# Kernel optimization log

Measured on AMD Instinct MI355X. Metric: run time of the kernel, lower is better.

Reference implementation:

```python
import jax, jax.numpy as jnp
import numpy as np

B, N, FIN, FOUT = 8, 2048, 128, 128


def setup_inputs() -> dict:
    key = jax.random.key(0)
    k1, k2, k3, k4, k5 = jax.random.split(key, 5)
    x = jax.random.normal(k1, (B, N, FIN), dtype=jnp.float32)
    adj = jax.random.randint(k2, (N, N), 0, 2, dtype=jnp.int32)
    # W stored [in, out] (transpose of torch Linear weight; same math via x @ W)
    W = jax.random.normal(k3, (FIN, FOUT), dtype=jnp.float32) * (1.0 / np.sqrt(FIN))
    # a: Linear(2*out, 1) split into src/dst halves: a([h_i,h_j]) = h_i@a_src + h_j@a_dst
    a_src = jax.random.normal(k4, (FOUT,), dtype=jnp.float32) * 0.1
    a_dst = jax.random.normal(k5, (FOUT,), dtype=jnp.float32) * 0.1
    return {"x": x, "adj": adj, "W": W, "a_src": a_src, "a_dst": a_dst}


def reference(x, adj, W, a_src, a_dst):
    # h: [B, N, FOUT]
    h = jnp.einsum('bnf,fo->bno', x, W)
    # attention logits e_ij = LeakyReLU(a_src.h_i + a_dst.h_j), built by broadcast
    s_i = jnp.einsum('bno,o->bn', h, a_src)  # [B, N]
    s_j = jnp.einsum('bno,o->bn', h, a_dst)  # [B, N]
    e = jax.nn.leaky_relu(s_i[:, :, None] + s_j[:, None, :], negative_slope=0.2)  # [B,N,N]
    scores = jnp.where(adj[None, :, :] == 0, -jnp.inf, e)
    attn = jax.nn.softmax(scores, axis=-1)
    attn = jnp.nan_to_num(attn, nan=0.0)  # rows with no neighbors -> all zeros
    # dropout is identity in eval mode
    out = jnp.einsum('bij,bjo->bio', attn, h)  # [B, N, FOUT]
    return out
```

## Files before the change

### kernel.cpp

```cpp
#include <hip/hip_runtime.h>
#include <math.h>

#define BATCH 8
#define NN 2048
#define FF 128

typedef __attribute__((ext_vector_type(4))) float f32x4;
typedef _Float16 half8 __attribute__((ext_vector_type(8)));

__device__ __forceinline__ unsigned short h2u(_Float16 h) {
    return __builtin_bit_cast(unsigned short, h);
}

__global__ __launch_bounds__(256) void k_h(const float* __restrict__ x,
                                           const int* __restrict__ adj,
                                           const float* __restrict__ W,
                                           const float* __restrict__ a_src,
                                           const float* __restrict__ a_dst,
                                           unsigned short* __restrict__ hF,
                                           float* __restrict__ Eg,  float* __restrict__ E2g,
                                           float* __restrict__ Sg,  float* __restrict__ S2g,
                                           unsigned* __restrict__ amT) {
    __shared__ float sred[4 * 16];
    __shared__ float dred[4 * 16];

    const int t = threadIdx.x;
    const int w = t >> 6, lane = t & 63;
    const int nl = lane & 15, quad = lane >> 4;
    const int row0 = blockIdx.x * 16;
    const int b = row0 >> 11, jloc0 = row0 & 2047;
    const int gr = row0 + nl;
    const int nt0 = w * 2;

    {
        const int prow = blockIdx.x * 2 + (w >> 1);
        const int* __restrict__ ar = adj + (size_t)prow * NN;
        const int s0 = (w & 1) * 16;
        #pragma unroll
        for (int s = 0; s < 16; ++s) {
            const int seg = s0 + s;
            const unsigned long long m = __ballot(ar[seg * 64 + lane] != 0);
            if (lane == 0)  amT[(size_t)(seg * 2) * NN + prow] = (unsigned)m;
            if (lane == 32) amT[(size_t)(seg * 2 + 1) * NN + prow] = (unsigned)(m >> 32);
        }
    }

    f32x4 acc[2] = {{0.f,0.f,0.f,0.f},{0.f,0.f,0.f,0.f}};

    #pragma unroll
    for (int ks = 0; ks < 4; ++ks) {
        const float4 xa = *reinterpret_cast<const float4*>(&x[(size_t)gr * FF + ks * 32 + quad * 8]);
        const float4 xb = *reinterpret_cast<const float4*>(&x[(size_t)gr * FF + ks * 32 + quad * 8 + 4]);
        const float xv[8] = {xa.x, xa.y, xa.z, xa.w, xb.x, xb.y, xb.z, xb.w};
        half8 ah, al;
        #pragma unroll
        for (int i = 0; i < 8; ++i) {
            const _Float16 hh = (_Float16)xv[i];
            ah[i] = hh;
            al[i] = (_Float16)(xv[i] - (float)hh);
        }
        #pragma unroll
        for (int nn = 0; nn < 2; ++nn) {
            const float* __restrict__ wp = W + (size_t)(ks * 32 + quad * 8) * FF + (nt0 + nn) * 16 + nl;
            half8 bh, bl;
            #pragma unroll
            for (int j = 0; j < 8; ++j) {
                const float wv = wp[j * FF];
                const _Float16 hh = (_Float16)wv;
                bh[j] = hh;
                bl[j] = (_Float16)(wv - (float)hh);
            }
            acc[nn] = __builtin_amdgcn_mfma_f32_16x16x32_f16(ah, bh, acc[nn], 0, 0, 0);
            acc[nn] = __builtin_amdgcn_mfma_f32_16x16x32_f16(al, bh, acc[nn], 0, 0, 0);
            acc[nn] = __builtin_amdgcn_mfma_f32_16x16x32_f16(ah, bl, acc[nn], 0, 0, 0);
        }
    }

    const int jloc = jloc0 + quad * 4;
    const int jg = jloc >> 3, u0 = jloc & 7;
    #pragma unroll
    for (int nn = 0; nn < 2; ++nn) {
        ushort4 hv;
        hv.x = h2u((_Float16)acc[nn][0]);
        hv.y = h2u((_Float16)acc[nn][1]);
        hv.z = h2u((_Float16)acc[nn][2]);
        hv.w = h2u((_Float16)acc[nn][3]);
        *reinterpret_cast<ushort4*>(&hF[(size_t)b * 262144 + (nt0 + nn) * 32768 + jg * 128 + nl * 8 + u0]) = hv;
    }

    float as[2], ad[2];
    #pragma unroll
    for (int nn = 0; nn < 2; ++nn) {
        const int col = (nt0 + nn) * 16 + nl;
        as[nn] = a_src[col];
        ad[nn] = a_dst[col];
    }
    #pragma unroll
    for (int r = 0; r < 4; ++r) {
        float sp = acc[0][r] * as[0] + acc[1][r] * as[1];
        float dp = acc[0][r] * ad[0] + acc[1][r] * ad[1];
        #pragma unroll
        for (int off = 8; off >= 1; off >>= 1) {
            sp += __shfl_xor(sp, off, 16);
            dp += __shfl_xor(dp, off, 16);
        }
        if (nl == 0) {
            sred[w * 16 + quad * 4 + r] = sp;
            dred[w * 16 + quad * 4 + r] = dp;
        }
    }
    __syncthreads();
    if (t < 16) {
        const float sp = sred[t] + sred[16 + t] + sred[32 + t] + sred[48 + t];
        const float dp = dred[t] + dred[16 + t] + dred[32 + t] + dred[48 + t];
        const int row = row0 + t;
        Sg[row]  = __expf(sp - 2.f);
        S2g[row] = __expf(0.2f * sp - 2.f);
        Eg[row]  = __expf(dp - 2.f);
        E2g[row] = __expf(0.2f * dp - 2.f);
    }
}

__global__ __launch_bounds__(512, 4) void k_attn(const unsigned short* __restrict__ hF,
                                                 const unsigned* __restrict__ amT,
                                                 const float* __restrict__ Eg,
                                                 const float* __restrict__ E2g,
                                                 const float* __restrict__ Sg,
                                                 const float* __restrict__ S2g,
                                                 float* __restrict__ P,
                                                 float* __restrict__ L) {
    __shared__ float E_l[512];
    __shared__ float E2_l[512];
    __shared__ unsigned am_l[16 * 64];
    __shared__ unsigned short pA[2 * 64 * 72];

    const int t = threadIdx.x;
    const int b = blockIdx.y;
    const int i0 = blockIdx.x * 64;
    const int jh = blockIdx.z;
    const int jbase = jh * 512;

    E_l[t]  = Eg[(size_t)b * NN + jbase + t];
    E2_l[t] = E2g[(size_t)b * NN + jbase + t];
    #pragma unroll
    for (int k = 0; k < 2; ++k) {
        const int idx = k * 512 + t;
        am_l[idx] = amT[(size_t)(jh * 16 + (idx >> 6)) * NN + i0 + (idx & 63)];
    }
    __syncthreads();

    const int rp = t >> 4, jw4 = t & 15;
    const int ra = rp * 2, rb = ra + 1;
    const float Sa  = Sg[(size_t)b * NN + i0 + ra];
    const float S2a = S2g[(size_t)b * NN + i0 + ra];
    const float Sb  = Sg[(size_t)b * NN + i0 + rb];
    const float S2b = S2g[(size_t)b * NN + i0 + rb];
    const int bitb = (jw4 & 7) * 4;
    const int pwo = ra * 72 + jw4 * 4;

    const int w = t >> 6, lane = t & 63;
    const int nl = lane & 15, quad = lane >> 4;
    const int mtp = w & 1, ntp = w >> 1;
    const unsigned short* __restrict__ hFb = hF + (size_t)b * 262144;
    int bofs[2], aofs[2];
    #pragma unroll
    for (int nn = 0; nn < 2; ++nn) bofs[nn] = (ntp + nn * 4) * 32768 + (jbase + quad * 8) * 16 + nl * 8;
    #pragma unroll
    for (int mm = 0; mm < 2; ++mm) aofs[mm] = ((mtp + mm * 2) * 16 + nl) * 72 + quad * 8;

    f32x4 acc[2][2] = {{{0.f,0.f,0.f,0.f},{0.f,0.f,0.f,0.f}},{{0.f,0.f,0.f,0.f},{0.f,0.f,0.f,0.f}}};
    f32x4 lac[2] = {{0.f,0.f,0.f,0.f},{0.f,0.f,0.f,0.f}};
    half8 ones;
    #pragma unroll
    for (int i = 0; i < 8; ++i) ones[i] = (_Float16)1.f;

    for (int tt = 0; tt < 8; ++tt) {
        const int buf = tt & 1;
        const int jofs = tt * 1024;

        half8 bfr[2][2];
        #pragma unroll
        for (int nn = 0; nn < 2; ++nn) {
            bfr[nn][0] = *reinterpret_cast<const half8*>(hFb + bofs[nn] + jofs);
            bfr[nn][1] = *reinterpret_cast<const half8*>(hFb + bofs[nn] + jofs + 512);
        }

        {
            const int jb = tt * 64 + jw4 * 4;
            const float4 ej4  = *reinterpret_cast<const float4*>(&E_l[jb]);
            const float4 e2j4 = *reinterpret_cast<const float4*>(&E2_l[jb]);
            const uint2 mw = *reinterpret_cast<const uint2*>(&am_l[(tt * 2 + (jw4 >> 3)) * 64 + ra]);
            const float ejA[4]  = {ej4.x, ej4.y, ej4.z, ej4.w};
            const float e2jA[4] = {e2j4.x, e2j4.y, e2j4.z, e2j4.w};
            ushort4 ha, hb;
            #pragma unroll
            for (int jj = 0; jj < 4; ++jj) {
                const float ua = fmaxf(Sa * ejA[jj], S2a * e2jA[jj]);
                const float ub = fmaxf(Sb * ejA[jj], S2b * e2jA[jj]);
                const float pa = ((mw.x >> (bitb + jj)) & 1u) ? ua : 0.f;
                const float pb = ((mw.y >> (bitb + jj)) & 1u) ? ub : 0.f;
                ((unsigned short*)&ha)[jj] = h2u((_Float16)pa);
                ((unsigned short*)&hb)[jj] = h2u((_Float16)pb);
            }
            *reinterpret_cast<ushort4*>(&pA[buf * 4608 + pwo]) = ha;
            *reinterpret_cast<ushort4*>(&pA[buf * 4608 + pwo + 72]) = hb;
        }

        __syncthreads();

        half8 afr[2][2];
        #pragma unroll
        for (int mm = 0; mm < 2; ++mm) {
            afr[mm][0] = *reinterpret_cast<const half8*>(&pA[buf * 4608 + aofs[mm]]);
            afr[mm][1] = *reinterpret_cast<const half8*>(&pA[buf * 4608 + aofs[mm] + 32]);
        }
        #pragma unroll
        for (int mm = 0; mm < 2; ++mm) {
            #pragma unroll
            for (int kh = 0; kh < 2; ++kh) {
                lac[mm] = __builtin_amdgcn_mfma_f32_16x16x32_f16(afr[mm][kh], ones, lac[mm], 0, 0, 0);
                acc[mm][0] = __builtin_amdgcn_mfma_f32_16x16x32_f16(afr[mm][kh], bfr[0][kh], acc[mm][0], 0, 0, 0);
                acc[mm][1] = __builtin_amdgcn_mfma_f32_16x16x32_f16(afr[mm][kh], bfr[1][kh], acc[mm][1], 0, 0, 0);
            }
        }
    }

    float* __restrict__ Pb = P + ((size_t)jh * BATCH + b) * 262144;
    float* __restrict__ Lb = L + ((size_t)jh * BATCH + b) * 2048;
    #pragma unroll
    for (int mm = 0; mm < 2; ++mm) {
        const int lrow = (mtp + mm * 2) * 16 + quad * 4;
        #pragma unroll
        for (int r = 0; r < 4; ++r) {
            #pragma unroll
            for (int nn = 0; nn < 2; ++nn) {
                const int col = (ntp + nn * 4) * 16 + nl;
                Pb[(size_t)(i0 + lrow + r) * FF + col] = acc[mm][nn][r];
            }
            if (nl == 0 && ntp == 0) Lb[i0 + lrow + r] = lac[mm][r];
        }
    }
}

__global__ __launch_bounds__(256) void k_comb(const float* __restrict__ P,
                                              const float* __restrict__ L,
                                              float* __restrict__ out) {
    const int g0 = blockIdx.x * 512 + threadIdx.x;
    #pragma unroll
    for (int it = 0; it < 2; ++it) {
        const int g = g0 + it * 256;
        const size_t flat = (size_t)g * 4;
        const int row = (int)(flat >> 7);
        const float l = L[row] + L[16384 + row] + L[32768 + row] + L[49152 + row];
        const float inv = (l > 0.f) ? 1.f / l : 0.f;
        const float4 p0 = *reinterpret_cast<const float4*>(&P[flat]);
        const float4 p1 = *reinterpret_cast<const float4*>(&P[2097152 + flat]);
        const float4 p2 = *reinterpret_cast<const float4*>(&P[4194304 + flat]);
        const float4 p3 = *reinterpret_cast<const float4*>(&P[6291456 + flat]);
        *reinterpret_cast<float4*>(&out[flat]) =
            make_float4((p0.x + p1.x + p2.x + p3.x) * inv,
                        (p0.y + p1.y + p2.y + p3.y) * inv,
                        (p0.z + p1.z + p2.z + p3.z) * inv,
                        (p0.w + p1.w + p2.w + p3.w) * inv);
    }
}

extern "C" void kernel_launch(void* const* d_in, const int* in_sizes, int n_in,
                              void* d_out, int out_size, void* d_ws, size_t ws_size,
                              hipStream_t stream) {
    const float* x     = (const float*)d_in[0];
    const int*   adj   = (const int*)d_in[1];
    const float* W     = (const float*)d_in[2];
    const float* a_src = (const float*)d_in[3];
    const float* a_dst = (const float*)d_in[4];
    float* out = (float*)d_out;

    unsigned short* hF = (unsigned short*)d_ws;
    float* Eg  = (float*)(hF + 2097152);
    float* E2g = Eg + 16384;
    float* Sg  = E2g + 16384;
    float* S2g = Sg + 16384;
    unsigned* amT = (unsigned*)(S2g + 16384);
    float* P = (float*)(amT + 131072);
    float* L = P + 8388608;

    k_h<<<1024, 256, 0, stream>>>(x, adj, W, a_src, a_dst, hF, Eg, E2g, Sg, S2g, amT);
    k_attn<<<dim3(32, BATCH, 4), 512, 0, stream>>>(hF, amT, Eg, E2g, Sg, S2g, P, L);
    k_comb<<<1024, 256, 0, stream>>>(P, L, out);
}
```

Baseline: 113.8 us.

## Halve the j-split, read E/mask from global, compute row sums with shuffles

The attention kernel now splits the neighbour dimension into 2 chunks instead of 4, so each block loops over 16 tiles, and the partial P/L buffers and the combine pass shrink to two slices. The LDS staging of E, E2 and the adjacency mask is dropped in favour of direct global loads inside the loop, which also removes the initial barrier. Row sums are accumulated in scalar registers and reduced with 16-lane shuffles instead of an extra MFMA against a ones vector. The trade-off is half as many blocks (512), giving less parallelism, plus global-load latency inside the loop.

```diff
diff --git a/kernel.cpp b/kernel.cpp
--- a/kernel.cpp
+++ b/kernel.cpp
@@ -129,25 +129,13 @@
                                                  const float* __restrict__ S2g,
                                                  float* __restrict__ P,
                                                  float* __restrict__ L) {
-    __shared__ float E_l[512];
-    __shared__ float E2_l[512];
-    __shared__ unsigned am_l[16 * 64];
     __shared__ unsigned short pA[2 * 64 * 72];
 
     const int t = threadIdx.x;
     const int b = blockIdx.y;
     const int i0 = blockIdx.x * 64;
     const int jh = blockIdx.z;
-    const int jbase = jh * 512;
-
-    E_l[t]  = Eg[(size_t)b * NN + jbase + t];
-    E2_l[t] = E2g[(size_t)b * NN + jbase + t];
-    #pragma unroll
-    for (int k = 0; k < 2; ++k) {
-        const int idx = k * 512 + t;
-        am_l[idx] = amT[(size_t)(jh * 16 + (idx >> 6)) * NN + i0 + (idx & 63)];
-    }
-    __syncthreads();
+    const int jbase = jh * 1024;
 
     const int rp = t >> 4, jw4 = t & 15;
     const int ra = rp * 2, rb = ra + 1;
@@ -157,6 +145,9 @@
     const float S2b = S2g[(size_t)b * NN + i0 + rb];
     const int bitb = (jw4 & 7) * 4;
     const int pwo = ra * 72 + jw4 * 4;
+    const float* __restrict__ Egb  = Eg  + (size_t)b * NN + jbase;
+    const float* __restrict__ E2gb = E2g + (size_t)b * NN + jbase;
+    const unsigned* __restrict__ amb = amT + (size_t)(jh * 32) * NN + i0;
 
     const int w = t >> 6, lane = t & 63;
     const int nl = lane & 15, quad = lane >> 4;
@@ -169,12 +160,9 @@
     for (int mm = 0; mm < 2; ++mm) aofs[mm] = ((mtp + mm * 2) * 16 + nl) * 72 + quad * 8;
 
     f32x4 acc[2][2] = {{{0.f,0.f,0.f,0.f},{0.f,0.f,0.f,0.f}},{{0.f,0.f,0.f,0.f},{0.f,0.f,0.f,0.f}}};
-    f32x4 lac[2] = {{0.f,0.f,0.f,0.f},{0.f,0.f,0.f,0.f}};
-    half8 ones;
-    #pragma unroll
-    for (int i = 0; i < 8; ++i) ones[i] = (_Float16)1.f;
-
-    for (int tt = 0; tt < 8; ++tt) {
+    float la = 0.f, lb = 0.f;
+
+    for (int tt = 0; tt < 16; ++tt) {
         const int buf = tt & 1;
         const int jofs = tt * 1024;
 
@@ -187,9 +175,9 @@
 
         {
             const int jb = tt * 64 + jw4 * 4;
-            const float4 ej4  = *reinterpret_cast<const float4*>(&E_l[jb]);
-            const float4 e2j4 = *reinterpret_cast<const float4*>(&E2_l[jb]);
-            const uint2 mw = *reinterpret_cast<const uint2*>(&am_l[(tt * 2 + (jw4 >> 3)) * 64 + ra]);
+            const float4 ej4  = *reinterpret_cast<const float4*>(&Egb[jb]);
+            const float4 e2j4 = *reinterpret_cast<const float4*>(&E2gb[jb]);
+            const uint2 mw = *reinterpret_cast<const uint2*>(&amb[(size_t)(tt * 2 + (jw4 >> 3)) * NN + ra]);
             const float ejA[4]  = {ej4.x, ej4.y, ej4.z, ej4.w};
             const float e2jA[4] = {e2j4.x, e2j4.y, e2j4.z, e2j4.w};
             ushort4 ha, hb;
@@ -199,6 +187,8 @@
                 const float ub = fmaxf(Sb * ejA[jj], S2b * e2jA[jj]);
                 const float pa = ((mw.x >> (bitb + jj)) & 1u) ? ua : 0.f;
                 const float pb = ((mw.y >> (bitb + jj)) & 1u) ? ub : 0.f;
+                la += pa;
+                lb += pb;
                 ((unsigned short*)&ha)[jj] = h2u((_Float16)pa);
                 ((unsigned short*)&hb)[jj] = h2u((_Float16)pb);
             }
@@ -218,15 +208,24 @@
         for (int mm = 0; mm < 2; ++mm) {
             #pragma unroll
             for (int kh = 0; kh < 2; ++kh) {
-                lac[mm] = __builtin_amdgcn_mfma_f32_16x16x32_f16(afr[mm][kh], ones, lac[mm], 0, 0, 0);
                 acc[mm][0] = __builtin_amdgcn_mfma_f32_16x16x32_f16(afr[mm][kh], bfr[0][kh], acc[mm][0], 0, 0, 0);
                 acc[mm][1] = __builtin_amdgcn_mfma_f32_16x16x32_f16(afr[mm][kh], bfr[1][kh], acc[mm][1], 0, 0, 0);
             }
         }
     }
 
+    #pragma unroll
+    for (int off = 8; off >= 1; off >>= 1) {
+        la += __shfl_xor(la, off, 16);
+        lb += __shfl_xor(lb, off, 16);
+    }
+
     float* __restrict__ Pb = P + ((size_t)jh * BATCH + b) * 262144;
     float* __restrict__ Lb = L + ((size_t)jh * BATCH + b) * 2048;
+    if (jw4 == 0) {
+        Lb[i0 + ra] = la;
+        Lb[i0 + rb] = lb;
+    }
     #pragma unroll
     for (int mm = 0; mm < 2; ++mm) {
         const int lrow = (mtp + mm * 2) * 16 + quad * 4;
@@ -237,7 +236,6 @@
                 const int col = (ntp + nn * 4) * 16 + nl;
                 Pb[(size_t)(i0 + lrow + r) * FF + col] = acc[mm][nn][r];
             }
-            if (nl == 0 && ntp == 0) Lb[i0 + lrow + r] = lac[mm][r];
         }
     }
 }
@@ -251,17 +249,13 @@
         const int g = g0 + it * 256;
         const size_t flat = (size_t)g * 4;
         const int row = (int)(flat >> 7);
-        const float l = L[row] + L[16384 + row] + L[32768 + row] + L[49152 + row];
+        const float l = L[row] + L[16384 + row];
         const float inv = (l > 0.f) ? 1.f / l : 0.f;
         const float4 p0 = *reinterpret_cast<const float4*>(&P[flat]);
         const float4 p1 = *reinterpret_cast<const float4*>(&P[2097152 + flat]);
-        const float4 p2 = *reinterpret_cast<const float4*>(&P[4194304 + flat]);
-        const float4 p3 = *reinterpret_cast<const float4*>(&P[6291456 + flat]);
         *reinterpret_cast<float4*>(&out[flat]) =
-            make_float4((p0.x + p1.x + p2.x + p3.x) * inv,
-                        (p0.y + p1.y + p2.y + p3.y) * inv,
-                        (p0.z + p1.z + p2.z + p3.z) * inv,
-                        (p0.w + p1.w + p2.w + p3.w) * inv);
+            make_float4((p0.x + p1.x) * inv, (p0.y + p1.y) * inv,
+                        (p0.z + p1.z) * inv, (p0.w + p1.w) * inv);
     }
 }
 
@@ -282,9 +276,9 @@
     float* S2g = Sg + 16384;
     unsigned* amT = (unsigned*)(S2g + 16384);
     float* P = (float*)(amT + 131072);
-    float* L = P + 8388608;
+    float* L = P + 4194304;
 
     k_h<<<1024, 256, 0, stream>>>(x, adj, W, a_src, a_dst, hF, Eg, E2g, Sg, S2g, amT);
-    k_attn<<<dim3(32, BATCH, 4), 512, 0, stream>>>(hF, amT, Eg, E2g, Sg, S2g, P, L);
+    k_attn<<<dim3(32, BATCH, 2), 512, 0, stream>>>(hF, amT, Eg, E2g, Sg, S2g, P, L);
     k_comb<<<1024, 256, 0, stream>>>(P, L, out);
 }
```

Result: no change. 113.0 us (median of 2 runs) (-0.7%).
